# Kernel tuning notes

Hardware: AMD Instinct MI355X
Metric: run time of the kernel (lower is better)

Reference implementation:

```python
import jax, jax.numpy as jnp
import numpy as np

N_NODES = 50000
N_EDGES = 800000
N_FEAT = 64
N_HID = 64
N_CLASSES = 10
N_GRAPHS = 64


def setup_inputs() -> dict:
    key = jax.random.key(0)
    ks = jax.random.split(key, 14)
    # edge_index with no self-loops (PyG add_remaining_self_loops then appends
    # exactly one self loop per node, which the reference reproduces)
    row = jax.random.randint(ks[0], (N_EDGES,), 0, N_NODES, dtype=jnp.int32)
    off = jax.random.randint(ks[1], (N_EDGES,), 1, N_NODES, dtype=jnp.int32)
    col = (row + off) % N_NODES
    edge_index = jnp.stack([row, col])
    batch = jnp.sort(jax.random.randint(ks[2], (N_NODES,), 0, N_GRAPHS, dtype=jnp.int32))
    x = jax.random.normal(ks[3], (N_NODES, N_FEAT), jnp.float32)
    P_vec = jax.random.normal(ks[4], (N_EDGES,), jnp.float32)

    def lin(k, fi, fo):
        return jax.random.normal(k, (fi, fo), jnp.float32) * (1.0 / np.sqrt(fi))

    return {
        "x": x, "edge_index": edge_index, "batch": batch, "P_vec": P_vec,
        "W1": lin(ks[5], N_FEAT, N_HID), "b1": jax.random.normal(ks[6], (N_HID,)) * 0.02,
        "W2": lin(ks[7], N_HID, N_HID), "b2": jax.random.normal(ks[8], (N_HID,)) * 0.02,
        "W3": lin(ks[9], N_HID, N_HID), "b3": jax.random.normal(ks[10], (N_HID,)) * 0.02,
        "Wl": lin(ks[11], N_HID, N_CLASSES), "bl": jax.random.normal(ks[12], (N_CLASSES,)) * 0.02,
    }


def reference(x, edge_index, batch, P_vec, W1, b1, W2, b2, W3, b3, Wl, bl):
    n = x.shape[0]
    row, col = edge_index[0], edge_index[1]
    # add_remaining_self_loops: append one self loop per node with weight 1.0
    sl = jnp.arange(n, dtype=row.dtype)
    fr = jnp.concatenate([row, sl])          # [E+N] source
    fc = jnp.concatenate([col, sl])          # [E+N] target (flow source_to_target)
    w = jnp.concatenate([jax.nn.sigmoid(P_vec), jnp.ones((n,), x.dtype)])
    deg = jax.ops.segment_sum(w, fc, num_segments=n)
    dis = jnp.where(deg > 0, deg ** -0.5, 0.0)  # deg_inv_sqrt, inf->0
    norm = dis[fr] * w * dis[fc]             # identical for all 3 conv layers

    def gcn_layer(h, W, b):
        h = h @ W                             # Linear (no bias inside lin)
        agg = jax.ops.segment_sum(norm[:, None] * h[fr], fc, num_segments=n)
        return agg + b

    h = jax.nn.relu(gcn_layer(x, W1, b1))
    h = jax.nn.relu(gcn_layer(h, W2, b2))
    h = gcn_layer(h, W3, b3)
    # global_mean_pool over batch segment ids
    sums = jax.ops.segment_sum(h, batch, num_segments=N_GRAPHS)
    cnt = jax.ops.segment_sum(jnp.ones((n, 1), h.dtype), batch, num_segments=N_GRAPHS)
    pooled = sums / jnp.maximum(cnt, 1.0)
    # dropout is identity at inference; final classifier
    return pooled @ Wl + bl
```

## Files before the change

### kernel.cpp

```cpp
#include <hip/hip_runtime.h>
#include <hip/hip_bf16.h>
#include <hip/hip_fp16.h>
#include <math.h>

#define N_GRAPHS 64
#define N_CLASSES 10
#define FIXSCALE 262144.0f
#define MAXDEG 64

typedef __hip_bfloat16 bf16;

__device__ __forceinline__ unsigned int pack_edge(int r, float s) {
    return ((unsigned int)r << 16) | (unsigned int)__half_as_ushort(__float2half(s));
}

__global__ void init_k(unsigned int* __restrict__ packed,
                       float* __restrict__ sums, float* __restrict__ cntG, int n) {
    int i = blockIdx.x * 256 + threadIdx.x;
    if (i < n) packed[i] = 0u;
    if (i < N_GRAPHS * 64) sums[i] = 0.0f;
    if (i < N_GRAPHS) cntG[i] = 0.0f;
}

__global__ void hist_k(const float* __restrict__ P, const int* __restrict__ row,
                       const int* __restrict__ col,
                       unsigned int* __restrict__ packed,
                       unsigned int* __restrict__ ell, int E) {
    int e = blockIdx.x * 256 + threadIdx.x;
    if (e < E) {
        float s = 1.0f / (1.0f + expf(-P[e]));
        unsigned int v = (1u << 24) | (unsigned int)(s * FIXSCALE + 0.5f);
        unsigned int old = atomicAdd(&packed[col[e]], v);
        unsigned int rank = old >> 24;
        if (rank < MAXDEG) ell[col[e] * MAXDEG + rank] = pack_edge(row[e], s);
    }
}

__global__ void disxg_k(const unsigned int* __restrict__ packed,
                        const float* __restrict__ x,
                        float* __restrict__ dis, bf16* __restrict__ xg,
                        unsigned int* __restrict__ ell, int n) {
    int i = blockIdx.x * 256 + threadIdx.x;
    if (i < n * 64) {
        int node = i >> 6;
        int lane = i & 63;
        unsigned int pk = packed[node];
        float deg = 1.0f + (float)(pk & 0xFFFFFFu) * (1.0f / FIXSCALE);
        float dv = 1.0f / sqrtf(deg);
        xg[i] = __float2bfloat16(x[i] * dv);
        if (lane == 0) dis[node] = dv;
        int cnt = (int)(pk >> 24);
        if (cnt > MAXDEG) cnt = MAXDEG;
        int pad = ((cnt + 15) & ~15) - cnt;
        if (lane < pad) ell[node * MAXDEG + cnt + lane] = 0u;
    }
}

__global__ void fold_k(const float* __restrict__ W3, const float* __restrict__ b3,
                       const float* __restrict__ Wl, const float* __restrict__ bl,
                       float* __restrict__ Wc, float* __restrict__ bc) {
    int t = blockIdx.x * 256 + threadIdx.x;
    if (t < 64 * N_CLASSES) {
        int k = t / N_CLASSES, c = t % N_CLASSES;
        float acc = 0.0f;
        for (int m = 0; m < 64; ++m) acc += W3[k * 64 + m] * Wl[m * N_CLASSES + c];
        Wc[t] = acc;
    }
    if (t < N_CLASSES) {
        float acc = bl[t];
        for (int m = 0; m < 64; ++m) acc += b3[m] * Wl[m * N_CLASSES + t];
        bc[t] = acc;
    }
}

__device__ __forceinline__ float edge_term(unsigned int v, const bf16* g, int lane) {
    int r = (int)(v >> 16);
    float s = __half2float(__ushort_as_half((unsigned short)(v & 0xFFFFu)));
    return s * __bfloat162float(g[r * 64 + lane]);
}

template <int MODE>
__global__ __launch_bounds__(256) void agg_mm_k(const bf16* __restrict__ g,
                                                const unsigned int* __restrict__ ell,
                                                const unsigned int* __restrict__ packed,
                                                const float* __restrict__ dis,
                                                const float* __restrict__ W,
                                                const float* __restrict__ b,
                                                float* __restrict__ out,
                                                bf16* __restrict__ out_bf, int n) {
    __shared__ float Wlds[MODE ? 64 * 64 : 1];
    int tid = threadIdx.x;
    if (MODE == 1) {
        for (int i = tid; i < 64 * 64; i += 256) Wlds[i] = W[i];
        __syncthreads();
    }
    int node = __builtin_amdgcn_readfirstlane(blockIdx.x * 4 + (tid >> 6));
    if (node >= n) return;
    int lane = tid & 63;

    float bv = (MODE == 1) ? b[lane] : 0.0f;
    float d = dis[node];
    int cnt = (int)(packed[node] >> 24);
    if (cnt > MAXDEG) cnt = MAXDEG;
    int cnt16 = (cnt + 15) & ~15;
    float acc = __bfloat162float(g[node * 64 + lane]);
    const unsigned int* rowp = ell + node * MAXDEG;

    float a[16];
#pragma unroll
    for (int t = 0; t < 16; ++t) a[t] = 0.0f;
    for (int j = 0; j < cnt16; j += 16) {
        unsigned int v[16];
#pragma unroll
        for (int t = 0; t < 16; ++t) v[t] = rowp[j + t];
#pragma unroll
        for (int t = 0; t < 16; ++t) a[t] += edge_term(v[t], g, lane);
    }
#pragma unroll
    for (int off = 8; off >= 1; off >>= 1)
#pragma unroll
        for (int t = 0; t < off; ++t) a[t] += a[t + off];
    acc += a[0];
    acc *= d;

    if (MODE == 1) {
        float o0 = bv, o1 = 0.f, o2 = 0.f, o3 = 0.f;
#pragma unroll
        for (int k = 0; k < 64; k += 4) {
            float av0 = __int_as_float(__builtin_amdgcn_readlane(__float_as_int(acc), k));
            float av1 = __int_as_float(__builtin_amdgcn_readlane(__float_as_int(acc), k + 1));
            float av2 = __int_as_float(__builtin_amdgcn_readlane(__float_as_int(acc), k + 2));
            float av3 = __int_as_float(__builtin_amdgcn_readlane(__float_as_int(acc), k + 3));
            o0 = fmaf(av0, Wlds[(k + 0) * 64 + lane], o0);
            o1 = fmaf(av1, Wlds[(k + 1) * 64 + lane], o1);
            o2 = fmaf(av2, Wlds[(k + 2) * 64 + lane], o2);
            o3 = fmaf(av3, Wlds[(k + 3) * 64 + lane], o3);
        }
        float o = fmaxf((o0 + o1) + (o2 + o3), 0.0f);
        out_bf[node * 64 + lane] = __float2bfloat16(d * o);
    } else {
        out[node * 64 + lane] = acc;
    }
}

__global__ __launch_bounds__(256) void poolpart_k(const float* __restrict__ h,
                                                  const int* __restrict__ batch,
                                                  float* __restrict__ sums,
                                                  float* __restrict__ cntG, int n) {
    int wave = threadIdx.x >> 6, lane = threadIdx.x & 63;
    int base = blockIdx.x * 128 + wave * 32;
    if (base >= n) return;
    int end = base + 32; if (end > n) end = n;
    int g = batch[base];
    float acc = 0.0f;
    int run = 0;
    for (int i = base; i < end; ++i) {
        int gi = batch[i];
        if (gi != g) {
            atomicAdd(&sums[g * 64 + lane], acc);
            if (lane == 0) atomicAdd(&cntG[g], (float)run);
            g = gi; acc = 0.0f; run = 0;
        }
        acc += h[i * 64 + lane];
        ++run;
    }
    atomicAdd(&sums[g * 64 + lane], acc);
    if (lane == 0) atomicAdd(&cntG[g], (float)run);
}

__global__ void classify_k(const float* __restrict__ sums, const float* __restrict__ cntG,
                           const float* __restrict__ Wc, const float* __restrict__ bc,
                           float* __restrict__ out) {
    __shared__ float pooled[64];
    int g = blockIdx.x;
    int t = threadIdx.x;
    float inv = 1.0f / fmaxf(cntG[g], 1.0f);
    pooled[t] = sums[g * 64 + t] * inv;
    __syncthreads();
    if (t < N_CLASSES) {
        float acc = bc[t];
        for (int k = 0; k < 64; ++k) acc += pooled[k] * Wc[k * N_CLASSES + t];
        out[g * N_CLASSES + t] = acc;
    }
}

extern "C" void kernel_launch(void* const* d_in, const int* in_sizes, int n_in,
                              void* d_out, int out_size, void* d_ws, size_t ws_size,
                              hipStream_t stream) {
    const float* x     = (const float*)d_in[0];
    const int*   eidx  = (const int*)d_in[1];
    const int*   batch = (const int*)d_in[2];
    const float* P     = (const float*)d_in[3];
    const float* W1 = (const float*)d_in[4];
    const float* b1 = (const float*)d_in[5];
    const float* W2 = (const float*)d_in[6];
    const float* b2 = (const float*)d_in[7];
    const float* W3 = (const float*)d_in[8];
    const float* b3 = (const float*)d_in[9];
    const float* Wl = (const float*)d_in[10];
    const float* bl = (const float*)d_in[11];
    float* out = (float*)d_out;

    const int N = in_sizes[2];
    const int E = in_sizes[3];
    const int* row = eidx;
    const int* col = eidx + E;

    char* p = (char*)d_ws;
    unsigned int* packed = (unsigned int*)p; p += (size_t)N * 4;
    float* dis      = (float*)p; p += (size_t)N * 4;
    float* sums     = (float*)p; p += (size_t)N_GRAPHS * 64 * 4;
    float* cntG     = (float*)p; p += (size_t)N_GRAPHS * 4;
    float* Wc       = (float*)p; p += (size_t)64 * N_CLASSES * 4;
    float* bc       = (float*)p; p += (size_t)N_CLASSES * 4;
    unsigned int* ell = (unsigned int*)p; p += (size_t)N * MAXDEG * 4;
    float* bufF     = (float*)p; p += (size_t)N * 64 * 4;
    bf16*  xg       = (bf16*)p;  p += (size_t)N * 64 * 2;
    bf16*  gA       = (bf16*)p;  p += (size_t)N * 64 * 2;
    bf16*  gB       = xg;

    dim3 blk(256);
    int nodeG = (N + 255) / 256;
    int edgeG = (E + 255) / 256;
    int bigG  = (N * 64 + 255) / 256;

    init_k<<<nodeG, blk, 0, stream>>>(packed, sums, cntG, N);
    hist_k<<<edgeG, blk, 0, stream>>>(P, row, col, packed, ell, E);
    disxg_k<<<bigG, blk, 0, stream>>>(packed, x, dis, xg, ell, N);
    fold_k<<<(64 * N_CLASSES + 255) / 256, blk, 0, stream>>>(W3, b3, Wl, bl, Wc, bc);

    int aggG = (N + 3) / 4;

    agg_mm_k<1><<<aggG, blk, 0, stream>>>(xg, ell, packed, dis, W1, b1, nullptr, gA, N);
    agg_mm_k<1><<<aggG, blk, 0, stream>>>(gA, ell, packed, dis, W2, b2, nullptr, gB, N);
    agg_mm_k<0><<<aggG, blk, 0, stream>>>(gB, ell, packed, dis, nullptr, nullptr, bufF, nullptr, N);

    int poolG = (N + 127) / 128;
    poolpart_k<<<poolG, blk, 0, stream>>>(bufF, batch, sums, cntG, N);
    classify_k<<<N_GRAPHS, dim3(64), 0, stream>>>(sums, cntG, Wc, bc, out);
}
```

Before: 262.5 us.

## Precompute packed edge records and bucket histogram scatter by target-node range

Sigmoid and edge packing move into the init kernel, which writes an interleaved record per edge into scratch space (reusing bufF). The histogram kernel then reads col and the records with vector loads, and each of 8 block groups handles only the edges whose target falls in its node range. This is meant to keep atomics and ELL writes within a smaller working set for better cache locality. In exchange, every block group rereads all edge data (8x read traffic), and the init kernel now launches E-sized grids and writes an extra buffer.

```diff
diff --git a/kernel.cpp b/kernel.cpp
--- a/kernel.cpp
+++ b/kernel.cpp
@@ -9,30 +9,66 @@
 #define MAXDEG 64
 
 typedef __hip_bfloat16 bf16;
+typedef int          i32x4 __attribute__((ext_vector_type(4)));
+typedef unsigned int u32x4 __attribute__((ext_vector_type(4)));
 
 __device__ __forceinline__ unsigned int pack_edge(int r, float s) {
     return ((unsigned int)r << 16) | (unsigned int)__half_as_ushort(__float2half(s));
 }
 
-__global__ void init_k(unsigned int* __restrict__ packed,
-                       float* __restrict__ sums, float* __restrict__ cntG, int n) {
+__global__ void init_k(const float* __restrict__ P, const int* __restrict__ row,
+                       unsigned int* __restrict__ packed, uint2* __restrict__ pre,
+                       float* __restrict__ sums, float* __restrict__ cntG,
+                       int n, int E) {
     int i = blockIdx.x * 256 + threadIdx.x;
     if (i < n) packed[i] = 0u;
     if (i < N_GRAPHS * 64) sums[i] = 0.0f;
     if (i < N_GRAPHS) cntG[i] = 0.0f;
-}
-
-__global__ void hist_k(const float* __restrict__ P, const int* __restrict__ row,
-                       const int* __restrict__ col,
-                       unsigned int* __restrict__ packed,
-                       unsigned int* __restrict__ ell, int E) {
-    int e = blockIdx.x * 256 + threadIdx.x;
-    if (e < E) {
-        float s = 1.0f / (1.0f + expf(-P[e]));
-        unsigned int v = (1u << 24) | (unsigned int)(s * FIXSCALE + 0.5f);
-        unsigned int old = atomicAdd(&packed[col[e]], v);
+    if (i < E) {
+        float s = 1.0f / (1.0f + expf(-P[i]));
+        pre[i] = make_uint2(pack_edge(row[i], s), (unsigned int)(s * FIXSCALE + 0.5f));
+    }
+}
+
+__device__ __forceinline__ void do_edge(int c, unsigned int rec, unsigned int fix, int myb,
+                                        unsigned int* __restrict__ packed,
+                                        unsigned int* __restrict__ ell) {
+    int b = (int)(((unsigned int)c * 41u) >> 18);
+    if (b > 7) b = 7;
+    if (b == myb) {
+        unsigned int old = atomicAdd(&packed[c], (1u << 24) | fix);
         unsigned int rank = old >> 24;
-        if (rank < MAXDEG) ell[col[e] * MAXDEG + rank] = pack_edge(row[e], s);
+        if (rank < MAXDEG) ell[c * MAXDEG + rank] = rec;
+    }
+}
+
+__global__ __launch_bounds__(256) void hist_k(const uint2* __restrict__ pre,
+                                              const int* __restrict__ col,
+                                              unsigned int* __restrict__ packed,
+                                              unsigned int* __restrict__ ell, int E) {
+    const int myb = blockIdx.x & 7;
+    const int slice = blockIdx.x >> 3;
+    const int E4 = E >> 2;
+    const i32x4* col4 = (const i32x4*)col;
+    const u32x4* pre4 = (const u32x4*)pre;
+#pragma unroll
+    for (int k = 0; k < 4; ++k) {
+        int i4 = slice * 1024 + k * 256 + (int)threadIdx.x;
+        if (i4 < E4) {
+            i32x4 c  = col4[i4];
+            u32x4 pa = pre4[2 * i4];
+            u32x4 pb = pre4[2 * i4 + 1];
+            do_edge(c[0], pa[0], pa[1], myb, packed, ell);
+            do_edge(c[1], pa[2], pa[3], myb, packed, ell);
+            do_edge(c[2], pb[0], pb[1], myb, packed, ell);
+            do_edge(c[3], pb[2], pb[3], myb, packed, ell);
+        }
+    }
+    if (slice == 0) {
+        for (int e = E4 * 4 + (int)threadIdx.x; e < E; e += 256) {
+            uint2 p = pre[e];
+            do_edge(col[e], p.x, p.y, myb, packed, ell);
+        }
     }
 }
 
@@ -207,25 +243,26 @@
     const int* col = eidx + E;
 
     char* p = (char*)d_ws;
+    unsigned int* ell = (unsigned int*)p; p += (size_t)N * MAXDEG * 4;
+    float* bufF     = (float*)p; p += (size_t)N * 64 * 4;
+    bf16*  xg       = (bf16*)p;  p += (size_t)N * 64 * 2;
+    bf16*  gA       = (bf16*)p;  p += (size_t)N * 64 * 2;
     unsigned int* packed = (unsigned int*)p; p += (size_t)N * 4;
     float* dis      = (float*)p; p += (size_t)N * 4;
     float* sums     = (float*)p; p += (size_t)N_GRAPHS * 64 * 4;
     float* cntG     = (float*)p; p += (size_t)N_GRAPHS * 4;
     float* Wc       = (float*)p; p += (size_t)64 * N_CLASSES * 4;
-    float* bc       = (float*)p; p += (size_t)N_CLASSES * 4;
-    unsigned int* ell = (unsigned int*)p; p += (size_t)N * MAXDEG * 4;
-    float* bufF     = (float*)p; p += (size_t)N * 64 * 4;
-    bf16*  xg       = (bf16*)p;  p += (size_t)N * 64 * 2;
-    bf16*  gA       = (bf16*)p;  p += (size_t)N * 64 * 2;
+    float* bc      = (float*)p; p += (size_t)N_CLASSES * 4;
     bf16*  gB       = xg;
+    uint2* pre      = (uint2*)bufF;
 
     dim3 blk(256);
-    int nodeG = (N + 255) / 256;
     int edgeG = (E + 255) / 256;
     int bigG  = (N * 64 + 255) / 256;
 
-    init_k<<<nodeG, blk, 0, stream>>>(packed, sums, cntG, N);
-    hist_k<<<edgeG, blk, 0, stream>>>(P, row, col, packed, ell, E);
+    init_k<<<edgeG, blk, 0, stream>>>(P, row, packed, pre, sums, cntG, N, E);
+    int nslice = ((E >> 2) + 1023) / 1024;
+    hist_k<<<nslice * 8, blk, 0, stream>>>(pre, col, packed, ell, E);
     disxg_k<<<bigG, blk, 0, stream>>>(packed, x, dis, xg, ell, N);
     fold_k<<<(64 * N_CLASSES + 255) / 256, blk, 0, stream>>>(W3, b3, Wl, bl, Wc, bc);
 
```

New measurement: 251.2 us. -4.3%, faster.

## Bin edges by destination range before CSR scatter; persistent grid for aggregation

Applied to the files above, without the earlier changes.

Edge preprocessing becomes two passes. The first kernel computes sigmoid weights and packed records, then appends each edge to one of 8 destination-range buckets using per-block LDS counters and one global atomic per bucket. A second kernel walks the buckets and does the degree atomics and ELL writes, aiming for better L2 locality on those atomics. The aggregation kernels switch to a fixed 1024-block grid-stride loop, so each block's load of W into LDS is amortised over many nodes. The price is an extra 16-byte-per-edge round trip through the bin buffer, and buckets have a fixed capacity that overflowing edges would silently exceed.

```diff
diff --git a/kernel.cpp b/kernel.cpp
--- a/kernel.cpp
+++ b/kernel.cpp
@@ -14,25 +14,66 @@
     return ((unsigned int)r << 16) | (unsigned int)__half_as_ushort(__float2half(s));
 }
 
-__global__ void init_k(unsigned int* __restrict__ packed,
-                       float* __restrict__ sums, float* __restrict__ cntG, int n) {
-    int i = blockIdx.x * 256 + threadIdx.x;
+__device__ __forceinline__ int bucket_of(int c) {
+    int b = (int)(((unsigned int)c * 41u) >> 18);
+    return b > 7 ? 7 : b;
+}
+
+__global__ __launch_bounds__(256) void init_k(const float* __restrict__ P,
+                                              const int* __restrict__ row,
+                                              const int* __restrict__ col,
+                                              unsigned int* __restrict__ packed,
+                                              uint4* __restrict__ binned,
+                                              unsigned int* __restrict__ gcnt,
+                                              float* __restrict__ sums,
+                                              float* __restrict__ cntG,
+                                              int n, int E, int capE) {
+    __shared__ unsigned int lcnt[8];
+    __shared__ unsigned int lbase[8];
+    int tid = threadIdx.x;
+    int i = blockIdx.x * 256 + tid;
+    if (tid < 8) lcnt[tid] = 0u;
     if (i < n) packed[i] = 0u;
     if (i < N_GRAPHS * 64) sums[i] = 0.0f;
     if (i < N_GRAPHS) cntG[i] = 0.0f;
-}
-
-__global__ void hist_k(const float* __restrict__ P, const int* __restrict__ row,
-                       const int* __restrict__ col,
-                       unsigned int* __restrict__ packed,
-                       unsigned int* __restrict__ ell, int E) {
-    int e = blockIdx.x * 256 + threadIdx.x;
-    if (e < E) {
-        float s = 1.0f / (1.0f + expf(-P[e]));
-        unsigned int v = (1u << 24) | (unsigned int)(s * FIXSCALE + 0.5f);
-        unsigned int old = atomicAdd(&packed[col[e]], v);
+    __syncthreads();
+
+    bool valid = (i < E);
+    int b = 0, c = 0;
+    unsigned int rec = 0, fix = 0, rank = 0;
+    if (valid) {
+        float s = 1.0f / (1.0f + expf(-P[i]));
+        rec = pack_edge(row[i], s);
+        fix = (unsigned int)(s * FIXSCALE + 0.5f);
+        c = col[i];
+        b = bucket_of(c);
+        rank = atomicAdd(&lcnt[b], 1u);
+    }
+    __syncthreads();
+    if (tid < 8 && lcnt[tid]) lbase[tid] = atomicAdd(&gcnt[tid], lcnt[tid]);
+    __syncthreads();
+    if (valid) {
+        unsigned int pos = lbase[b] + rank;
+        if (pos < (unsigned int)capE)
+            binned[(size_t)b * capE + pos] = make_uint4(rec, fix, (unsigned int)c, 0u);
+    }
+}
+
+__global__ __launch_bounds__(256) void scatter_k(const uint4* __restrict__ binned,
+                                                 const unsigned int* __restrict__ gcnt,
+                                                 unsigned int* __restrict__ packed,
+                                                 unsigned int* __restrict__ ell, int capE) {
+    const int myb = blockIdx.x & 7;
+    const int sub = blockIdx.x >> 3;
+    const int nsub = gridDim.x >> 3;
+    unsigned int cnt = gcnt[myb];
+    if (cnt > (unsigned int)capE) cnt = (unsigned int)capE;
+    const uint4* bin = binned + (size_t)myb * capE;
+    for (unsigned int i = sub * 256u + threadIdx.x; i < cnt; i += (unsigned int)nsub * 256u) {
+        uint4 r = bin[i];
+        unsigned int old = atomicAdd(&packed[r.z], (1u << 24) | r.y);
         unsigned int rank = old >> 24;
-        if (rank < MAXDEG) ell[col[e] * MAXDEG + rank] = pack_edge(row[e], s);
+        if (rank < MAXDEG) ell[r.z * MAXDEG + rank] = r.x;
     }
 }
 
@@ -94,52 +135,55 @@
         for (int i = tid; i < 64 * 64; i += 256) Wlds[i] = W[i];
         __syncthreads();
     }
-    int node = __builtin_amdgcn_readfirstlane(blockIdx.x * 4 + (tid >> 6));
-    if (node >= n) return;
     int lane = tid & 63;
-
     float bv = (MODE == 1) ? b[lane] : 0.0f;
-    float d = dis[node];
-    int cnt = (int)(packed[node] >> 24);
-    if (cnt > MAXDEG) cnt = MAXDEG;
-    int cnt16 = (cnt + 15) & ~15;
-    float acc = __bfloat162float(g[node * 64 + lane]);
-    const unsigned int* rowp = ell + node * MAXDEG;
-
-    float a[16];
-#pragma unroll
-    for (int t = 0; t < 16; ++t) a[t] = 0.0f;
-    for (int j = 0; j < cnt16; j += 16) {
-        unsigned int v[16];
-#pragma unroll
-        for (int t = 0; t < 16; ++t) v[t] = rowp[j + t];
-#pragma unroll
-        for (int t = 0; t < 16; ++t) a[t] += edge_term(v[t], g, lane);
-    }
-#pragma unroll
-    for (int off = 8; off >= 1; off >>= 1)
-#pragma unroll
-        for (int t = 0; t < off; ++t) a[t] += a[t + off];
-    acc += a[0];
-    acc *= d;
-
-    if (MODE == 1) {
-        float o0 = bv, o1 = 0.f, o2 = 0.f, o3 = 0.f;
-#pragma unroll
-        for (int k = 0; k < 64; k += 4) {
-            float av0 = __int_as_float(__builtin_amdgcn_readlane(__float_as_int(acc), k));
-            float av1 = __int_as_float(__builtin_amdgcn_readlane(__float_as_int(acc), k + 1));
-            float av2 = __int_as_float(__builtin_amdgcn_readlane(__float_as_int(acc), k + 2));
-            float av3 = __int_as_float(__builtin_amdgcn_readlane(__float_as_int(acc), k + 3));
-            o0 = fmaf(av0, Wlds[(k + 0) * 64 + lane], o0);
-            o1 = fmaf(av1, Wlds[(k + 1) * 64 + lane], o1);
-            o2 = fmaf(av2, Wlds[(k + 2) * 64 + lane], o2);
-            o3 = fmaf(av3, Wlds[(k + 3) * 64 + lane], o3);
+
+    for (int base = blockIdx.x * 4; base < n; base += gridDim.x * 4) {
+        int node = __builtin_amdgcn_readfirstlane(base + (tid >> 6));
+        if (node >= n) continue;
+
+        float d = dis[node];
+        int cnt = (int)(packed[node] >> 24);
+        if (cnt > MAXDEG) cnt = MAXDEG;
+        int cnt16 = (cnt + 15) & ~15;
+        float acc = __bfloat162float(g[node * 64 + lane]);
+        const unsigned int* rowp = ell + node * MAXDEG;
+
+        float a[16];
+#pragma unroll
+        for (int t = 0; t < 16; ++t) a[t] = 0.0f;
+        for (int j = 0; j < cnt16; j += 16) {
+            unsigned int v[16];
+#pragma unroll
+            for (int t = 0; t < 16; ++t) v[t] = rowp[j + t];
+#pragma unroll
+            for (int t = 0; t < 16; ++t) a[t] += edge_term(v[t], g, lane);
         }
-        float o = fmaxf((o0 + o1) + (o2 + o3), 0.0f);
-        out_bf[node * 64 + lane] = __float2bfloat16(d * o);
-    } else {
-        out[node * 64 + lane] = acc;
+#pragma unroll
+        for (int off = 8; off >= 1; off >>= 1)
+#pragma unroll
+            for (int t = 0; t < off; ++t) a[t] += a[t + off];
+        acc += a[0];
+        acc *= d;
+
+        if (MODE == 1) {
+            float o0 = bv, o1 = 0.f, o2 = 0.f, o3 = 0.f;
+#pragma unroll
+            for (int k = 0; k < 64; k += 4) {
+                float av0 = __int_as_float(__builtin_amdgcn_readlane(__float_as_int(acc), k));
+                float av1 = __int_as_float(__builtin_amdgcn_readlane(__float_as_int(acc), k + 1));
+                float av2 = __int_as_float(__builtin_amdgcn_readlane(__float_as_int(acc), k + 2));
+                float av3 = __int_as_float(__builtin_amdgcn_readlane(__float_as_int(acc), k + 3));
+                o0 = fmaf(av0, Wlds[(k + 0) * 64 + lane], o0);
+                o1 = fmaf(av1, Wlds[(k + 1) * 64 + lane], o1);
+                o2 = fmaf(av2, Wlds[(k + 2) * 64 + lane], o2);
+                o3 = fmaf(av3, Wlds[(k + 3) * 64 + lane], o3);
+            }
+            float o = fmaxf((o0 + o1) + (o2 + o3), 0.0f);
+            out_bf[node * 64 + lane] = __float2bfloat16(d * o);
+        } else {
+            out[node * 64 + lane] = acc;
+        }
     }
 }
 
@@ -205,31 +249,34 @@
     const int E = in_sizes[3];
     const int* row = eidx;
     const int* col = eidx + E;
+    const int capE = E / 8 + 8192;
 
     char* p = (char*)d_ws;
+    unsigned int* ell = (unsigned int*)p; p += (size_t)N * MAXDEG * 4;
+    float* bufF     = (float*)p; p += (size_t)N * 64 * 4;
+    bf16*  xg       = (bf16*)p;  p += (size_t)N * 64 * 2;
+    bf16*  gA       = (bf16*)p;  p += (size_t)N * 64 * 2;
+    uint4* binned   = (uint4*)p; p += (size_t)8 * capE * 16;
     unsigned int* packed = (unsigned int*)p; p += (size_t)N * 4;
     float* dis      = (float*)p; p += (size_t)N * 4;
     float* sums     = (float*)p; p += (size_t)N_GRAPHS * 64 * 4;
     float* cntG     = (float*)p; p += (size_t)N_GRAPHS * 4;
     float* Wc       = (float*)p; p += (size_t)64 * N_CLASSES * 4;
     float* bc       = (float*)p; p += (size_t)N_CLASSES * 4;
-    unsigned int* ell = (unsigned int*)p; p += (size_t)N * MAXDEG * 4;
-    float* bufF     = (float*)p; p += (size_t)N * 64 * 4;
-    bf16*  xg       = (bf16*)p;  p += (size_t)N * 64 * 2;
-    bf16*  gA       = (bf16*)p;  p += (size_t)N * 64 * 2;
+    unsigned int* gcnt = (unsigned int*)p; p += 8 * 4;
     bf16*  gB       = xg;
 
     dim3 blk(256);
-    int nodeG = (N + 255) / 256;
     int edgeG = (E + 255) / 256;
     int bigG  = (N * 64 + 255) / 256;
 
-    init_k<<<nodeG, blk, 0, stream>>>(packed, sums, cntG, N);
-    hist_k<<<edgeG, blk, 0, stream>>>(P, row, col, packed, ell, E);
+    hipMemsetAsync(gcnt, 0, 8 * sizeof(unsigned int), stream);
+    init_k<<<edgeG, blk, 0, stream>>>(P, row, col, packed, binned, gcnt, sums, cntG, N, E, capE);
+    scatter_k<<<768, blk, 0, stream>>>(binned, gcnt, packed, ell, capE);
     disxg_k<<<bigG, blk, 0, stream>>>(packed, x, dis, xg, ell, N);
     fold_k<<<(64 * N_CLASSES + 255) / 256, blk, 0, stream>>>(W3, b3, Wl, bl, Wc, bc);
 
-    int aggG = (N + 3) / 4;
+    int aggG = 1024;
 
     agg_mm_k<1><<<aggG, blk, 0, stream>>>(xg, ell, packed, dis, W1, b1, nullptr, gA, N);
     agg_mm_k<1><<<aggG, blk, 0, stream>>>(gA, ell, packed, dis, W2, b2, nullptr, gB, N);
```

Result: slower. 291.1 us (+10.9%).
